# Performance work log

Hardware: AMD Instinct MI355X
Metric: run time of the kernel (lower is better)

## Reference

```python
import jax, jax.numpy as jnp
import numpy as np

B, S, H, E = 2, 2048, 16, 64
INV_SCALE = 8.0  # sqrt(head_dim); forward divides scores by this


def setup_inputs() -> dict:
    key = jax.random.key(0)
    ks = jax.random.split(key, 10)
    return {
        "query": jax.random.normal(ks[0], (B, S, H, E), dtype=jnp.float32),
        "key": jax.random.normal(ks[1], (B, S, H, E), dtype=jnp.float32),
        "value": jax.random.normal(ks[2], (B, S, H, E), dtype=jnp.float32),
        "attn_mask": jax.random.randint(ks[3], (B, S), 0, 2, dtype=jnp.int32),
        "Wq": jax.random.normal(ks[4], (E, E), dtype=jnp.float32) / np.sqrt(E),
        "bq": jax.random.normal(ks[5], (E,), dtype=jnp.float32) * 0.02,
        "Wk": jax.random.normal(ks[6], (E, E), dtype=jnp.float32) / np.sqrt(E),
        "bk": jax.random.normal(ks[7], (E,), dtype=jnp.float32) * 0.02,
        "Wv": jax.random.normal(ks[8], (E, E), dtype=jnp.float32) / np.sqrt(E),
        "bv": jax.random.normal(ks[9], (E,), dtype=jnp.float32) * 0.02,
    }


def reference(query, key, value, attn_mask, Wq, bq, Wk, bk, Wv, bv):
    # Linear projections over the last (embed) dim; torch Linear: x @ W.T + b
    q = jnp.einsum('bshe,fe->bhsf', query, Wq) + bq  # [B,H,S,E] (permute 0,2,1,3 fused)
    k = jnp.einsum('bshe,fe->bhsf', key, Wk) + bk
    v = jnp.einsum('bshe,fe->bhsf', value, Wv) + bv
    scores = jnp.einsum('bhqe,bhke->bhqk', q, k) / INV_SCALE  # [B,H,S,S]
    # mask: positions where attn_mask == 0 get -inf, broadcast over (1,1,k_len)
    masked = attn_mask[:, None, None, :] == 0  # [B,1,1,S]
    scores = jnp.where(masked, -jnp.inf, scores)
    attn = jax.nn.softmax(scores, axis=-1)
    out = jnp.einsum('bhqk,bhke->bqhe', attn, v)  # permute back to [B,S,H,E]
    return out
```

## Files before the change

### kernel.cpp

```cpp
#include <hip/hip_runtime.h>


#define BATCH 2
#define SEQ   2048
#define NH    16
#define DE    64
#define LDP   72
#define LDOF  68
#define NKT   (SEQ / 64)
#define LOG2E 1.44269504088896340736f
#define CSHIFT 16.0f

using bf16x8   = __attribute__((ext_vector_type(8))) __bf16;
using bf16x4   = __attribute__((ext_vector_type(4))) __bf16;
using floatx4  = __attribute__((ext_vector_type(4))) float;
using ushortx4 = __attribute__((ext_vector_type(4))) unsigned short;
using ushortx8 = __attribute__((ext_vector_type(8))) unsigned short;

__device__ __forceinline__ ushortx4 cvt4(floatx4 f) {
    bf16x4 h = __builtin_convertvector(f, bf16x4);
    return __builtin_bit_cast(ushortx4, h);
}

__device__ __forceinline__ void glds16(const unsigned short* g, unsigned short* l) {
    __builtin_amdgcn_global_load_lds(
        (const __attribute__((address_space(1))) unsigned int*)g,
        (__attribute__((address_space(3))) unsigned int*)l, 16, 0, 0);
}

__global__ __launch_bounds__(256) void proj_kernel(
    const float* __restrict__ xq, const float* __restrict__ xk, const float* __restrict__ xv,
    const float* __restrict__ Wq, const float* __restrict__ bq,
    const float* __restrict__ Wk, const float* __restrict__ bk,
    const float* __restrict__ Wv, const float* __restrict__ bv,
    unsigned short* __restrict__ qb, unsigned short* __restrict__ kb,
    unsigned short* __restrict__ vtb)
{
    __shared__ __align__(16) unsigned short Xb[64 * LDP];
    __shared__ __align__(16) unsigned short Wb[64 * LDP];
    __shared__ __align__(16) unsigned short Ob[64 * LDP];
    __shared__ float blds[64];

    const int t  = threadIdx.x;
    const int p  = blockIdx.x >> 10;
    const int bh = (blockIdx.x >> 5) & 31;
    const int st = blockIdx.x & 31;
    const int s0 = st * 64;
    const int b  = bh >> 4, h = bh & 15;
    const int lane = t & 63, w = t >> 6, quad = lane >> 4, l16 = lane & 15;

    const float* x    = (p == 0) ? xq : (p == 1) ? xk : xv;
    const float* W    = (p == 0) ? Wq : (p == 1) ? Wk : Wv;
    const float* bias = (p == 0) ? bq : (p == 1) ? bk : bv;

    #pragma unroll
    for (int i = 0; i < 4; ++i) {
        int idx = i * 1024 + t * 4;
        int row = idx >> 6, col = idx & 63;
        floatx4 xv4 = *(const floatx4*)(x + (((size_t)(b * SEQ + s0 + row) * NH + h) * DE + col));
        *(ushortx4*)&Xb[row * LDP + col] = cvt4(xv4);
        floatx4 wv4 = *(const floatx4*)(W + row * 64 + col);
        *(ushortx4*)&Wb[row * LDP + col] = cvt4(wv4);
    }
    if (t < 64) blds[t] = bias[t];
    __syncthreads();

    if (p < 2) {
        bf16x8 a0 = *(const bf16x8*)&Wb[(w * 16 + l16) * LDP + quad * 8];
        bf16x8 a1 = *(const bf16x8*)&Wb[(w * 16 + l16) * LDP + 32 + quad * 8];
        floatx4 bf4 = *(const floatx4*)&blds[w * 16 + quad * 4];
        const float scale = (p == 0) ? 0.125f * LOG2E : 1.0f;
        #pragma unroll
        for (int nb = 0; nb < 4; ++nb) {
            bf16x8 b0 = *(const bf16x8*)&Xb[(nb * 16 + l16) * LDP + quad * 8];
            bf16x8 b1 = *(const bf16x8*)&Xb[(nb * 16 + l16) * LDP + 32 + quad * 8];
            floatx4 c = {0.f, 0.f, 0.f, 0.f};
            c = __builtin_amdgcn_mfma_f32_16x16x32_bf16(a0, b0, c, 0, 0, 0);
            c = __builtin_amdgcn_mfma_f32_16x16x32_bf16(a1, b1, c, 0, 0, 0);
            floatx4 v;
            v[0] = (c[0] + bf4[0]) * scale; v[1] = (c[1] + bf4[1]) * scale;
            v[2] = (c[2] + bf4[2]) * scale; v[3] = (c[3] + bf4[3]) * scale;
            *(ushortx4*)&Ob[(nb * 16 + l16) * LDP + w * 16 + quad * 4] = cvt4(v);
        }
    } else {
        bf16x8 a0 = *(const bf16x8*)&Xb[(w * 16 + l16) * LDP + quad * 8];
        bf16x8 a1 = *(const bf16x8*)&Xb[(w * 16 + l16) * LDP + 32 + quad * 8];
        #pragma unroll
        for (int nb = 0; nb < 4; ++nb) {
            bf16x8 b0 = *(const bf16x8*)&Wb[(nb * 16 + l16) * LDP + quad * 8];
            bf16x8 b1 = *(const bf16x8*)&Wb[(nb * 16 + l16) * LDP + 32 + quad * 8];
            floatx4 c = {0.f, 0.f, 0.f, 0.f};
            c = __builtin_amdgcn_mfma_f32_16x16x32_bf16(a0, b0, c, 0, 0, 0);
            c = __builtin_amdgcn_mfma_f32_16x16x32_bf16(a1, b1, c, 0, 0, 0);
            float bw = blds[nb * 16 + l16];
            floatx4 v;
            v[0] = c[0] + bw; v[1] = c[1] + bw; v[2] = c[2] + bw; v[3] = c[3] + bw;
            *(ushortx4*)&Ob[(nb * 16 + l16) * LDP + w * 16 + quad * 4] = cvt4(v);
        }
    }
    __syncthreads();

    #pragma unroll
    for (int j = 0; j < 2; ++j) {
        int idx = j * 256 + t;
        int row = idx >> 3, c = idx & 7;
        int cp  = (c ^ (row & 7)) * 8;
        ushortx8 v = *(const ushortx8*)&Ob[row * LDP + c * 8];
        if (p < 2) {
            unsigned short* dst = (p == 0) ? qb : kb;
            *(ushortx8*)(dst + ((size_t)bh * SEQ + s0 + row) * DE + cp) = v;
        } else {
            *(ushortx8*)(vtb + ((size_t)bh * DE + row) * SEQ + s0 + cp) = v;
        }
    }
}

__global__ __launch_bounds__(512) void attn_kernel(
    const unsigned short* __restrict__ qb, const unsigned short* __restrict__ kb,
    const unsigned short* __restrict__ vtb, const int* __restrict__ mask,
    float* __restrict__ out)
{
    __shared__ __align__(16) char smem[16384 + 16384 + 18432 + 512];
    unsigned short* Kl = (unsigned short*)smem;
    unsigned short* Vl = (unsigned short*)(smem + 16384);
    unsigned short* Pq = (unsigned short*)(smem + 32768);
    float*          Ml = (float*)(smem + 32768 + 18432);
    float*          Ol = (float*)smem;

    const int t  = threadIdx.x;
    const int qt = blockIdx.x, bh = blockIdx.y;
    const int b  = bh >> 4, h = bh & 15;
    const int q0 = qt * 128;
    const int lane = t & 63, w = t >> 6;
    const int quad = lane >> 4, l16 = lane & 15;
    const int cS = ((quad ^ (l16 & 7)) * 8);

    const unsigned short* kbase = kb + (size_t)bh * SEQ * DE;
    const unsigned short* vbase = vtb + (size_t)bh * DE * SEQ;
    const unsigned short* qsrc  = qb + ((size_t)bh * SEQ + q0) * DE;
    const int* mrow = mask + b * SEQ;

    glds16(qsrc + (w * 16) * DE + lane * 8,      Pq + (w * 16) * 64);
    glds16(qsrc + (w * 16 + 8) * DE + lane * 8,  Pq + (w * 16 + 8) * 64);
    glds16(kbase + (size_t)(w * 8) * DE + lane * 8, Kl + w * 512);
    glds16(vbase + (size_t)(w * 8 + (lane >> 3)) * SEQ + (lane & 7) * 8, Vl + w * 512);
    if (t < 64) Ml[t] = mrow[t] ? 0.f : -1e30f;
    int mreg = (t < 64) ? mrow[64 + t] : 0;
    __syncthreads();

    bf16x8 qf0 = *(const bf16x8*)&Pq[(w * 16 + l16) * 64 + cS];
    bf16x8 qf1 = *(const bf16x8*)&Pq[(w * 16 + l16) * 64 + (cS ^ 32)];

    bf16x8 onesf;
    #pragma unroll
    for (int i = 0; i < 8; ++i) onesf[i] = (__bf16)1.0f;

    floatx4 o[4], acc_l;
    #pragma unroll
    for (int nb = 0; nb < 4; ++nb) o[nb] = floatx4{0.f, 0.f, 0.f, 0.f};
    acc_l = floatx4{0.f, 0.f, 0.f, 0.f};

    for (int kt = 0; kt < NKT; ++kt) {
        const int cur = kt & 1, nxt = cur ^ 1;
        const unsigned short* Kc = Kl + cur * 4096;
        const unsigned short* Vc = Vl + cur * 4096;
        const float*          Mc = Ml + cur * 64;

        if (kt + 1 < NKT) {
            const int k1 = (kt + 1) * 64;
            glds16(kbase + (size_t)(k1 + w * 8) * DE + lane * 8, Kl + nxt * 4096 + w * 512);
            glds16(vbase + (size_t)(w * 8 + (lane >> 3)) * SEQ + k1 + (lane & 7) * 8,
                   Vl + nxt * 4096 + w * 512);
            if (t < 64) Ml[nxt * 64 + t] = mreg ? 0.f : -1e30f;
            mreg = (t < 64 && kt + 2 < NKT) ? mrow[(kt + 2) * 64 + t] : 0;
        }

        floatx4 sc[4];
        #pragma unroll
        for (int sub = 0; sub < 4; ++sub) {
            const int r = sub * 16 + l16;
            bf16x8 kf0 = *(const bf16x8*)&Kc[r * 64 + cS];
            bf16x8 kf1 = *(const bf16x8*)&Kc[r * 64 + (cS ^ 32)];
            floatx4 c = *(const floatx4*)&Mc[sub * 16 + quad * 4];
            c = __builtin_amdgcn_mfma_f32_16x16x32_bf16(kf0, qf0, c, 0, 0, 0);
            c = __builtin_amdgcn_mfma_f32_16x16x32_bf16(kf1, qf1, c, 0, 0, 0);
            sc[sub] = c;
        }

        #pragma unroll
        for (int sub = 0; sub < 4; ++sub) {
            #pragma unroll
            for (int r = 0; r < 4; ++r)
                sc[sub][r] = __builtin_amdgcn_exp2f(sc[sub][r] - CSHIFT);
            *(ushortx4*)&Pq[(w * 16 + l16) * LDP + sub * 16 + quad * 4] = cvt4(sc[sub]);
        }
        __asm__ volatile("s_waitcnt lgkmcnt(0)" ::: "memory");

        bf16x8 pf0 = *(const bf16x8*)&Pq[(w * 16 + l16) * LDP + quad * 8];
        bf16x8 pf1 = *(const bf16x8*)&Pq[(w * 16 + l16) * LDP + 32 + quad * 8];
        #pragma unroll
        for (int nb = 0; nb < 4; ++nb) {
            const int r = nb * 16 + l16;
            bf16x8 vf0 = *(const bf16x8*)&Vc[r * 64 + cS];
            bf16x8 vf1 = *(const bf16x8*)&Vc[r * 64 + (cS ^ 32)];
            o[nb] = __builtin_amdgcn_mfma_f32_16x16x32_bf16(vf0, pf0, o[nb], 0, 0, 0);
            o[nb] = __builtin_amdgcn_mfma_f32_16x16x32_bf16(vf1, pf1, o[nb], 0, 0, 0);
        }
        acc_l = __builtin_amdgcn_mfma_f32_16x16x32_bf16(onesf, pf0, acc_l, 0, 0, 0);
        acc_l = __builtin_amdgcn_mfma_f32_16x16x32_bf16(onesf, pf1, acc_l, 0, 0, 0);

        __syncthreads();
    }

    float invl = __builtin_amdgcn_rcpf(acc_l[0]);
    #pragma unroll
    for (int nb = 0; nb < 4; ++nb) {
        floatx4 ov;
        ov[0] = o[nb][0] * invl; ov[1] = o[nb][1] * invl;
        ov[2] = o[nb][2] * invl; ov[3] = o[nb][3] * invl;
        *(floatx4*)&Ol[(w * 16 + l16) * LDOF + nb * 16 + quad * 4] = ov;
    }
    __asm__ volatile("s_waitcnt lgkmcnt(0)" ::: "memory");
    #pragma unroll
    for (int pass = 0; pass < 4; ++pass) {
        int rl  = w * 16 + pass * 4 + quad;
        int col = l16 * 4;
        floatx4 tv = *(const floatx4*)&Ol[rl * LDOF + col];
        *(floatx4*)(out + (((size_t)b * SEQ + q0 + rl) * NH + h) * DE + col) = tv;
    }
}

extern "C" void kernel_launch(void* const* d_in, const int* in_sizes, int n_in,
                              void* d_out, int out_size, void* d_ws, size_t ws_size,
                              hipStream_t stream) {
    const float* query = (const float*)d_in[0];
    const float* key   = (const float*)d_in[1];
    const float* value = (const float*)d_in[2];
    const int*   mask  = (const int*)d_in[3];
    const float* Wq = (const float*)d_in[4];
    const float* bq = (const float*)d_in[5];
    const float* Wk = (const float*)d_in[6];
    const float* bk = (const float*)d_in[7];
    const float* Wv = (const float*)d_in[8];
    const float* bv = (const float*)d_in[9];

    const size_t tensor_elems = (size_t)BATCH * NH * SEQ * DE;
    unsigned short* qb  = (unsigned short*)d_ws;
    unsigned short* kb  = qb + tensor_elems;
    unsigned short* vtb = kb + tensor_elems;

    proj_kernel<<<dim3(3 * BATCH * NH * (SEQ / 64)), 256, 0, stream>>>(
        query, key, value, Wq, bq, Wk, bk, Wv, bv, qb, kb, vtb);
    attn_kernel<<<dim3(SEQ / 128, BATCH * NH), 512, 0, stream>>>(
        qb, kb, vtb, mask, (float*)d_out);
}
```

Before: 154.3 us.

## Switch attention to 32x32x16 MFMA with 32 query rows per wave

Restructures the attention kernel so each of 4 waves owns 32 query rows and uses 32x32x16 bf16 MFMA for both QK^T and PV, replacing 16x16x32 tiles spread over 8 waves. The softmax row sum now comes from VALU adds plus a lane shuffle rather than an extra MFMA against a ones vector, and the constant shift is folded into the mask bias. The goal is fewer MFMA issues, fewer LDS fragment loads per FLOP and no wasted MFMA for the row sum, at the cost of more registers per wave and half the threads per block.

```diff
diff --git a/kernel.cpp b/kernel.cpp
--- a/kernel.cpp
+++ b/kernel.cpp
@@ -9,11 +9,11 @@
 #define LDOF  68
 #define NKT   (SEQ / 64)
 #define LOG2E 1.44269504088896340736f
-#define CSHIFT 16.0f
 
 using bf16x8   = __attribute__((ext_vector_type(8))) __bf16;
 using bf16x4   = __attribute__((ext_vector_type(4))) __bf16;
 using floatx4  = __attribute__((ext_vector_type(4))) float;
+using floatx16 = __attribute__((ext_vector_type(16))) float;
 using ushortx4 = __attribute__((ext_vector_type(4))) unsigned short;
 using ushortx8 = __attribute__((ext_vector_type(8))) unsigned short;
 
@@ -115,16 +115,16 @@
     }
 }
 
-__global__ __launch_bounds__(512) void attn_kernel(
+__global__ __launch_bounds__(256) void attn_kernel(
     const unsigned short* __restrict__ qb, const unsigned short* __restrict__ kb,
     const unsigned short* __restrict__ vtb, const int* __restrict__ mask,
     float* __restrict__ out)
 {
-    __shared__ __align__(16) char smem[16384 + 16384 + 18432 + 512];
+    __shared__ __align__(16) char smem[16384 * 3 + 512];
     unsigned short* Kl = (unsigned short*)smem;
     unsigned short* Vl = (unsigned short*)(smem + 16384);
     unsigned short* Pq = (unsigned short*)(smem + 32768);
-    float*          Ml = (float*)(smem + 32768 + 18432);
+    float*          Ml = (float*)(smem + 49152);
     float*          Ol = (float*)smem;
 
     const int t  = threadIdx.x;
@@ -132,33 +132,38 @@
     const int b  = bh >> 4, h = bh & 15;
     const int q0 = qt * 128;
     const int lane = t & 63, w = t >> 6;
-    const int quad = lane >> 4, l16 = lane & 15;
-    const int cS = ((quad ^ (l16 & 7)) * 8);
+    const int l31 = lane & 31, hl = lane >> 5;
+    const int sw  = l31 & 7;
+    const int qrow = w * 32 + l31;
 
     const unsigned short* kbase = kb + (size_t)bh * SEQ * DE;
     const unsigned short* vbase = vtb + (size_t)bh * DE * SEQ;
     const unsigned short* qsrc  = qb + ((size_t)bh * SEQ + q0) * DE;
     const int* mrow = mask + b * SEQ;
 
-    glds16(qsrc + (w * 16) * DE + lane * 8,      Pq + (w * 16) * 64);
-    glds16(qsrc + (w * 16 + 8) * DE + lane * 8,  Pq + (w * 16 + 8) * 64);
-    glds16(kbase + (size_t)(w * 8) * DE + lane * 8, Kl + w * 512);
-    glds16(vbase + (size_t)(w * 8 + (lane >> 3)) * SEQ + (lane & 7) * 8, Vl + w * 512);
-    if (t < 64) Ml[t] = mrow[t] ? 0.f : -1e30f;
+    #pragma unroll
+    for (int u = 0; u < 4; ++u)
+        glds16(qsrc + (w * 32 + u * 8 + (lane >> 3)) * DE + (lane & 7) * 8,
+               Pq + (w * 32 + u * 8) * 64);
+    glds16(kbase + (size_t)(w * 16 + (lane >> 3)) * DE + (lane & 7) * 8,     Kl + w * 1024);
+    glds16(kbase + (size_t)(w * 16 + 8 + (lane >> 3)) * DE + (lane & 7) * 8, Kl + w * 1024 + 512);
+    glds16(vbase + (size_t)(w * 16 + (lane >> 3)) * SEQ + (lane & 7) * 8,     Vl + w * 1024);
+    glds16(vbase + (size_t)(w * 16 + 8 + (lane >> 3)) * SEQ + (lane & 7) * 8, Vl + w * 1024 + 512);
+    if (t < 64) Ml[t] = mrow[t] ? -16.0f : -1e30f;
     int mreg = (t < 64) ? mrow[64 + t] : 0;
     __syncthreads();
 
-    bf16x8 qf0 = *(const bf16x8*)&Pq[(w * 16 + l16) * 64 + cS];
-    bf16x8 qf1 = *(const bf16x8*)&Pq[(w * 16 + l16) * 64 + (cS ^ 32)];
-
-    bf16x8 onesf;
-    #pragma unroll
-    for (int i = 0; i < 8; ++i) onesf[i] = (__bf16)1.0f;
-
-    floatx4 o[4], acc_l;
-    #pragma unroll
-    for (int nb = 0; nb < 4; ++nb) o[nb] = floatx4{0.f, 0.f, 0.f, 0.f};
-    acc_l = floatx4{0.f, 0.f, 0.f, 0.f};
+    bf16x8 qf[4];
+    #pragma unroll
+    for (int estep = 0; estep < 4; ++estep)
+        qf[estep] = *(const bf16x8*)&Pq[qrow * 64 + ((2 * estep + hl) ^ sw) * 8];
+
+    float l_i = 0.f;
+    floatx16 oacc[2];
+    #pragma unroll
+    for (int eh = 0; eh < 2; ++eh)
+        #pragma unroll
+        for (int r = 0; r < 16; ++r) oacc[eh][r] = 0.f;
 
     for (int kt = 0; kt < NKT; ++kt) {
         const int cur = kt & 1, nxt = cur ^ 1;
@@ -168,63 +173,80 @@
 
         if (kt + 1 < NKT) {
             const int k1 = (kt + 1) * 64;
-            glds16(kbase + (size_t)(k1 + w * 8) * DE + lane * 8, Kl + nxt * 4096 + w * 512);
-            glds16(vbase + (size_t)(w * 8 + (lane >> 3)) * SEQ + k1 + (lane & 7) * 8,
-                   Vl + nxt * 4096 + w * 512);
-            if (t < 64) Ml[nxt * 64 + t] = mreg ? 0.f : -1e30f;
+            glds16(kbase + (size_t)(k1 + w * 16 + (lane >> 3)) * DE + (lane & 7) * 8,
+                   Kl + nxt * 4096 + w * 1024);
+            glds16(kbase + (size_t)(k1 + w * 16 + 8 + (lane >> 3)) * DE + (lane & 7) * 8,
+                   Kl + nxt * 4096 + w * 1024 + 512);
+            glds16(vbase + (size_t)(w * 16 + (lane >> 3)) * SEQ + k1 + (lane & 7) * 8,
+                   Vl + nxt * 4096 + w * 1024);
+            glds16(vbase + (size_t)(w * 16 + 8 + (lane >> 3)) * SEQ + k1 + (lane & 7) * 8,
+                   Vl + nxt * 4096 + w * 1024 + 512);
+            if (t < 64) Ml[nxt * 64 + t] = mreg ? -16.0f : -1e30f;
             mreg = (t < 64 && kt + 2 < NKT) ? mrow[(kt + 2) * 64 + t] : 0;
         }
 
-        floatx4 sc[4];
-        #pragma unroll
-        for (int sub = 0; sub < 4; ++sub) {
-            const int r = sub * 16 + l16;
-            bf16x8 kf0 = *(const bf16x8*)&Kc[r * 64 + cS];
-            bf16x8 kf1 = *(const bf16x8*)&Kc[r * 64 + (cS ^ 32)];
-            floatx4 c = *(const floatx4*)&Mc[sub * 16 + quad * 4];
-            c = __builtin_amdgcn_mfma_f32_16x16x32_bf16(kf0, qf0, c, 0, 0, 0);
-            c = __builtin_amdgcn_mfma_f32_16x16x32_bf16(kf1, qf1, c, 0, 0, 0);
-            sc[sub] = c;
-        }
-
-        #pragma unroll
-        for (int sub = 0; sub < 4; ++sub) {
-            #pragma unroll
-            for (int r = 0; r < 4; ++r)
-                sc[sub][r] = __builtin_amdgcn_exp2f(sc[sub][r] - CSHIFT);
-            *(ushortx4*)&Pq[(w * 16 + l16) * LDP + sub * 16 + quad * 4] = cvt4(sc[sub]);
-        }
+        float sum = 0.f;
+        #pragma unroll
+        for (int kh = 0; kh < 2; ++kh) {
+            floatx16 c;
+            #pragma unroll
+            for (int g = 0; g < 4; ++g) {
+                floatx4 mg = *(const floatx4*)&Mc[kh * 32 + g * 8 + hl * 4];
+                c[g * 4 + 0] = mg[0]; c[g * 4 + 1] = mg[1];
+                c[g * 4 + 2] = mg[2]; c[g * 4 + 3] = mg[3];
+            }
+            #pragma unroll
+            for (int estep = 0; estep < 4; ++estep) {
+                bf16x8 kf = *(const bf16x8*)&Kc[(kh * 32 + l31) * 64 + ((2 * estep + hl) ^ sw) * 8];
+                c = __builtin_amdgcn_mfma_f32_32x32x16_bf16(kf, qf[estep], c, 0, 0, 0);
+            }
+            #pragma unroll
+            for (int r = 0; r < 16; ++r) {
+                c[r] = __builtin_amdgcn_exp2f(c[r]);
+                sum += c[r];
+            }
+            #pragma unroll
+            for (int m = 0; m < 4; ++m) {
+                floatx4 g4 = {c[4 * m + 0], c[4 * m + 1], c[4 * m + 2], c[4 * m + 3]};
+                *(ushortx4*)&Pq[qrow * 64 + (((m + 4 * kh) ^ sw) * 8) + hl * 4] = cvt4(g4);
+            }
+        }
+        sum += __shfl_xor(sum, 32);
+        l_i += sum;
         __asm__ volatile("s_waitcnt lgkmcnt(0)" ::: "memory");
 
-        bf16x8 pf0 = *(const bf16x8*)&Pq[(w * 16 + l16) * LDP + quad * 8];
-        bf16x8 pf1 = *(const bf16x8*)&Pq[(w * 16 + l16) * LDP + 32 + quad * 8];
-        #pragma unroll
-        for (int nb = 0; nb < 4; ++nb) {
-            const int r = nb * 16 + l16;
-            bf16x8 vf0 = *(const bf16x8*)&Vc[r * 64 + cS];
-            bf16x8 vf1 = *(const bf16x8*)&Vc[r * 64 + (cS ^ 32)];
-            o[nb] = __builtin_amdgcn_mfma_f32_16x16x32_bf16(vf0, pf0, o[nb], 0, 0, 0);
-            o[nb] = __builtin_amdgcn_mfma_f32_16x16x32_bf16(vf1, pf1, o[nb], 0, 0, 0);
-        }
-        acc_l = __builtin_amdgcn_mfma_f32_16x16x32_bf16(onesf, pf0, acc_l, 0, 0, 0);
-        acc_l = __builtin_amdgcn_mfma_f32_16x16x32_bf16(onesf, pf1, acc_l, 0, 0, 0);
+        bf16x8 pf[4];
+        #pragma unroll
+        for (int kstep = 0; kstep < 4; ++kstep)
+            pf[kstep] = *(const bf16x8*)&Pq[qrow * 64 + ((2 * kstep + hl) ^ sw) * 8];
+
+        #pragma unroll
+        for (int eh = 0; eh < 2; ++eh)
+            #pragma unroll
+            for (int kstep = 0; kstep < 4; ++kstep) {
+                bf16x8 vf = *(const bf16x8*)&Vc[(eh * 32 + l31) * 64 + ((2 * kstep + hl) ^ sw) * 8];
+                oacc[eh] = __builtin_amdgcn_mfma_f32_32x32x16_bf16(vf, pf[kstep], oacc[eh], 0, 0, 0);
+            }
 
         __syncthreads();
     }
 
-    float invl = __builtin_amdgcn_rcpf(acc_l[0]);
-    #pragma unroll
-    for (int nb = 0; nb < 4; ++nb) {
-        floatx4 ov;
-        ov[0] = o[nb][0] * invl; ov[1] = o[nb][1] * invl;
-        ov[2] = o[nb][2] * invl; ov[3] = o[nb][3] * invl;
-        *(floatx4*)&Ol[(w * 16 + l16) * LDOF + nb * 16 + quad * 4] = ov;
-    }
-    __asm__ volatile("s_waitcnt lgkmcnt(0)" ::: "memory");
-    #pragma unroll
-    for (int pass = 0; pass < 4; ++pass) {
-        int rl  = w * 16 + pass * 4 + quad;
-        int col = l16 * 4;
+    __syncthreads();
+    float invl = __builtin_amdgcn_rcpf(l_i);
+    #pragma unroll
+    for (int eh = 0; eh < 2; ++eh)
+        #pragma unroll
+        for (int m = 0; m < 4; ++m) {
+            floatx4 ov;
+            ov[0] = oacc[eh][4 * m + 0] * invl; ov[1] = oacc[eh][4 * m + 1] * invl;
+            ov[2] = oacc[eh][4 * m + 2] * invl; ov[3] = oacc[eh][4 * m + 3] * invl;
+            *(floatx4*)&Ol[qrow * LDOF + eh * 32 + m * 8 + hl * 4] = ov;
+        }
+    __syncthreads();
+    #pragma unroll
+    for (int pass = 0; pass < 8; ++pass) {
+        int rl  = pass * 16 + (t >> 4);
+        int col = (t & 15) * 4;
         floatx4 tv = *(const floatx4*)&Ol[rl * LDOF + col];
         *(floatx4*)(out + (((size_t)b * SEQ + q0 + rl) * NH + h) * DE + col) = tv;
     }
@@ -251,6 +273,6 @@
 
     proj_kernel<<<dim3(3 * BATCH * NH * (SEQ / 64)), 256, 0, stream>>>(
         query, key, value, Wq, bq, Wk, bk, Wv, bv, qb, kb, vtb);
-    attn_kernel<<<dim3(SEQ / 128, BATCH * NH), 512, 0, stream>>>(
+    attn_kernel<<<dim3(SEQ / 128, BATCH * NH), 256, 0, stream>>>(
         qb, kb, vtb, mask, (float*)d_out);
 }
```

Measured after the change: 163.6 us. 6.0% more time.
